# Optimization experiments

Measured on AMD Instinct MI355X. Metric: run time of the kernel, lower is better.

The kernel has to match this reference:

```python
import jax, jax.numpy as jnp
import numpy as np

B, S, DIM = 4, 2048, 1024


def _xavier(key, shape):
    # xavier_uniform for a [out, in] Linear weight
    fan_in, fan_out = shape[1], shape[0]
    limit = float(np.sqrt(6.0 / (fan_in + fan_out)))
    return jax.random.uniform(key, shape, jnp.float32, -limit, limit)


def setup_inputs() -> dict:
    key = jax.random.key(0)
    ks = jax.random.split(key, 8)
    z_real = jax.random.normal(ks[0], (B, S, DIM), jnp.float32)
    z_imag = jax.random.normal(ks[1], (B, S, DIM), jnp.float32)
    wq_r = _xavier(ks[2], (DIM, DIM))
    wq_i = _xavier(ks[3], (DIM, DIM))
    wk_r = _xavier(ks[4], (DIM, DIM))
    wk_i = _xavier(ks[5], (DIM, DIM))
    wv_r = _xavier(ks[6], (DIM, DIM))
    wv_i = _xavier(ks[7], (DIM, DIM))
    # causal mask (0 = masked), broadcast over batch
    mask = jnp.tril(jnp.ones((S, S), jnp.int32))
    return {"z_real": z_real, "z_imag": z_imag,
            "wq_r": wq_r, "wq_i": wq_i,
            "wk_r": wk_r, "wk_i": wk_i,
            "wv_r": wv_r, "wv_i": wv_i,
            "mask": mask}


def _complex_linear(xr, xi, wr, wi):
    # torch Linear: y = x @ W^T
    yr = xr @ wr.T - xi @ wi.T
    yi = xi @ wr.T + xr @ wi.T
    return yr, yi


def reference(z_real, z_imag, wq_r, wq_i, wk_r, wk_i, wv_r, wv_i, mask):
    dim = z_real.shape[-1]
    scale = dim ** (-0.5)
    qr, qi = _complex_linear(z_real, z_imag, wq_r, wq_i)
    kr, ki = _complex_linear(z_real, z_imag, wk_r, wk_i)
    vr, vi = _complex_linear(z_real, z_imag, wv_r, wv_i)
    # cat([q.real, q.imag]) @ cat([k.real, k.imag])^T == qr@kr^T + qi@ki^T
    scores = (jnp.einsum('bsd,btd->bst', qr, kr)
              + jnp.einsum('bsd,btd->bst', qi, ki)) * scale  # [B,S,S]
    scores = jnp.where(mask == 0, -jnp.inf, scores)
    attn = jax.nn.softmax(scores, axis=-1)
    out_r = jnp.einsum('bst,btd->bsd', attn, vr)
    out_i = jnp.einsum('bst,btd->bsd', attn, vi)
    return jnp.stack([out_r, out_i], axis=0)  # [2,B,S,dim] = (real, imag)
```

## Files before the change

kernel.cpp:

```cpp
#include <hip/hip_runtime.h>
#include <hip/hip_bf16.h>
#include <hip/hip_fp16.h>

#define DIMK 1024
#define SEQ  2048
#define BATCH 4
#define NTOK (BATCH*SEQ)
#define PROJ_ELEMS ((size_t)NTOK*DIMK)
#define LD 2048

typedef unsigned short ushort_t;
typedef __attribute__((ext_vector_type(8))) short short8;
typedef __attribute__((ext_vector_type(4))) float float4v;

#define MFMA_BF16 __builtin_amdgcn_mfma_f32_16x16x32_bf16

__device__ __forceinline__ unsigned short f2bf(float f) {
    union { float f; unsigned int i; } x; x.f = f;
    unsigned int r = x.i + 0x7fffu + ((x.i >> 16) & 1u);
    return (unsigned short)(r >> 16);
}

__device__ __forceinline__ void gld_lds16(const void* g, void* l) {
    auto gp = reinterpret_cast<const __attribute__((address_space(1))) unsigned int*>(
        reinterpret_cast<uintptr_t>(g));
    auto lp = reinterpret_cast<__attribute__((address_space(3))) unsigned int*>(
        reinterpret_cast<uintptr_t>(l));
    __builtin_amdgcn_global_load_lds(gp, lp, 16, 0, 0);
}

__device__ __forceinline__ void stage2(const ushort_t* __restrict__ gbase,
                                       ushort_t* lbase, int kcol,
                                       int rg0, int g, int scol)
{
    gld_lds16(gbase + (size_t)(rg0 * 16 + g) * LD + kcol + scol,
              lbase + rg0 * 512);
    gld_lds16(gbase + (size_t)(rg0 * 16 + 16 + g) * LD + kcol + scol,
              lbase + rg0 * 512 + 512);
}

__device__ __forceinline__ void gemm_core256(
    const ushort_t* __restrict__ Arow,
    const ushort_t* __restrict__ Brow,
    int kend,
    ushort_t* Alds, ushort_t* Blds,
    float4v acc[8][4], int wid, int lane)
{
    const int g    = lane >> 2;
    const int sx   = lane & 3;
    const int scol = ((sx - (g >> 1)) & 3) * 8;
    const int r16  = lane & 15;
    const int quad = lane >> 4;
    const int roff = r16 * 32 + ((quad + (r16 >> 1)) & 3) * 8;
    const int wm8 = (wid >> 2) * 8;
    const int wn4 = (wid & 3) * 4;
    const int rg0 = wid * 2;
    const int NT = kend >> 6;

    stage2(Brow, Blds,        0,  rg0, g, scol);
    stage2(Arow, Alds,        0,  rg0, g, scol);
    stage2(Brow, Blds + 8192, 32, rg0, g, scol);
    stage2(Arow, Alds + 8192, 32, rg0, g, scol);
    asm volatile("s_waitcnt vmcnt(4)" ::: "memory");
    __builtin_amdgcn_s_barrier();

    for (int t = 0; t < NT; ++t) {
        const int d     = (t & 1) << 14;
        const int dn    = d ^ 16384;
        const int knext = (t + 1) << 6;
        const bool pre  = (t + 1 < NT);
        short8 af0[4], af1[4], bf[4];

        #pragma unroll
        for (int j = 0; j < 4; ++j)
            bf[j] = *(const short8*)(Blds + d + (wn4 + j) * 512 + roff);
        #pragma unroll
        for (int i = 0; i < 4; ++i)
            af0[i] = *(const short8*)(Alds + d + (wm8 + i) * 512 + roff);
        #pragma unroll
        for (int i = 0; i < 4; ++i)
            af1[i] = *(const short8*)(Alds + d + (wm8 + 4 + i) * 512 + roff);
        if (pre) {
            stage2(Brow, Blds + dn, knext, rg0, g, scol);
            stage2(Arow, Alds + dn, knext, rg0, g, scol);
        }
        __builtin_amdgcn_s_setprio(1);
        #pragma unroll
        for (int i = 0; i < 4; ++i)
            #pragma unroll
            for (int j = 0; j < 4; ++j)
                acc[i][j] = MFMA_BF16(af0[i], bf[j], acc[i][j], 0, 0, 0);
        #pragma unroll
        for (int i = 0; i < 4; ++i)
            #pragma unroll
            for (int j = 0; j < 4; ++j)
                acc[4 + i][j] = MFMA_BF16(af1[i], bf[j], acc[4 + i][j], 0, 0, 0);
        __builtin_amdgcn_s_setprio(0);
        if (pre) asm volatile("s_waitcnt vmcnt(4)" ::: "memory");
        else     asm volatile("s_waitcnt vmcnt(0)" ::: "memory");
        __builtin_amdgcn_s_barrier();

        #pragma unroll
        for (int j = 0; j < 4; ++j)
            bf[j] = *(const short8*)(Blds + d + 8192 + (wn4 + j) * 512 + roff);
        #pragma unroll
        for (int i = 0; i < 4; ++i)
            af0[i] = *(const short8*)(Alds + d + 8192 + (wm8 + i) * 512 + roff);
        #pragma unroll
        for (int i = 0; i < 4; ++i)
            af1[i] = *(const short8*)(Alds + d + 8192 + (wm8 + 4 + i) * 512 + roff);
        if (pre) {
            stage2(Brow, Blds + dn + 8192, knext + 32, rg0, g, scol);
            stage2(Arow, Alds + dn + 8192, knext + 32, rg0, g, scol);
        }
        __builtin_amdgcn_s_setprio(1);
        #pragma unroll
        for (int i = 0; i < 4; ++i)
            #pragma unroll
            for (int j = 0; j < 4; ++j)
                acc[i][j] = MFMA_BF16(af0[i], bf[j], acc[i][j], 0, 0, 0);
        #pragma unroll
        for (int i = 0; i < 4; ++i)
            #pragma unroll
            for (int j = 0; j < 4; ++j)
                acc[4 + i][j] = MFMA_BF16(af1[i], bf[j], acc[4 + i][j], 0, 0, 0);
        __builtin_amdgcn_s_setprio(0);
        if (pre) asm volatile("s_waitcnt vmcnt(4)" ::: "memory");
        __builtin_amdgcn_s_barrier();
    }
}

__global__ __launch_bounds__(512, 2)
void gemm_proj(const ushort_t* __restrict__ A, const ushort_t* __restrict__ B,
               ushort_t* __restrict__ Cq, ushort_t* __restrict__ Ck,
               ushort_t* __restrict__ Cv)
{
    __shared__ ushort_t smem[65536];
    const int tid = threadIdx.x, wid = tid >> 6, lane = tid & 63;
    const int m0 = blockIdx.y * 256;
    const int n0g = blockIdx.x * 256;
    ushort_t* C = (n0g < 2048) ? Cq : ((n0g < 4096) ? Ck : Cv);
    const int n0 = n0g & 2047;
    float4v acc[8][4] = {};
    gemm_core256(A + (size_t)m0 * LD, B + (size_t)n0g * LD, 2048,
                 smem, smem + 32768, acc, wid, lane);

    const int wm = wid >> 2, wn = wid & 3;
    const int col16 = lane & 15, quad = lane >> 4;
    #pragma unroll
    for (int i = 0; i < 8; ++i)
        #pragma unroll
        for (int j = 0; j < 4; ++j) {
            const int n = n0 + wn * 64 + j * 16 + col16;
            #pragma unroll
            for (int r = 0; r < 4; ++r) {
                const int m = m0 + wm * 128 + i * 16 + quad * 4 + r;
                C[(size_t)m * LD + n] = f2bf(acc[i][j][r]);
            }
        }
}

__global__ __launch_bounds__(512, 2)
void gemm_scores(const ushort_t* __restrict__ Q, const ushort_t* __restrict__ K,
                 __half* __restrict__ S)
{
    const int jt = blockIdx.x, it = blockIdx.y, b = blockIdx.z;
    if (jt > it) return;
    __shared__ ushort_t smem[65536];
    const int tid = threadIdx.x, wid = tid >> 6, lane = tid & 63;
    const size_t boff = (size_t)b * SEQ * LD;
    float4v acc[8][4] = {};
    gemm_core256(Q + boff + (size_t)it * 256 * LD, K + boff + (size_t)jt * 256 * LD,
                 2048, smem, smem + 32768, acc, wid, lane);

    const int wm = wid >> 2, wn = wid & 3;
    const int col16 = lane & 15, quad = lane >> 4;
    const float scale = 0.03125f;
    __half* Sb = S + (size_t)b * SEQ * SEQ;
    #pragma unroll
    for (int i = 0; i < 8; ++i)
        #pragma unroll
        for (int j = 0; j < 4; ++j) {
            const int t = jt * 256 + wn * 64 + j * 16 + col16;
            #pragma unroll
            for (int r = 0; r < 4; ++r) {
                const int s = it * 256 + wm * 128 + i * 16 + quad * 4 + r;
                Sb[(size_t)s * SEQ + t] = __float2half(acc[i][j][r] * scale);
            }
        }
}

__global__ __launch_bounds__(512, 2)
void gemm_pv(const ushort_t* __restrict__ P, const ushort_t* __restrict__ VT,
             float* __restrict__ out)
{
    const int nt = blockIdx.x, mt = blockIdx.y, b = blockIdx.z;
    __shared__ ushort_t smem[65536];
    const int tid = threadIdx.x, wid = tid >> 6, lane = tid & 63;
    const int kend = (mt + 1) * 256;
    float4v acc[8][4] = {};
    gemm_core256(P + (size_t)b * SEQ * SEQ + (size_t)mt * 256 * LD,
                 VT + (size_t)b * LD * LD + (size_t)nt * 256 * LD,
                 kend, smem, smem + 32768, acc, wid, lane);

    const int wm = wid >> 2, wn = wid & 3;
    const int col16 = lane & 15, quad = lane >> 4;
    #pragma unroll
    for (int i = 0; i < 8; ++i)
        #pragma unroll
        for (int j = 0; j < 4; ++j) {
            const int n = nt * 256 + wn * 64 + j * 16 + col16;
            float* dst = out + ((n < 1024) ? 0 : PROJ_ELEMS);
            const int d = n & 1023;
            #pragma unroll
            for (int r = 0; r < 4; ++r) {
                const int s = mt * 256 + wm * 128 + i * 16 + quad * 4 + r;
                dst[((size_t)b * SEQ + s) * DIMK + d] = acc[i][j][r];
            }
        }
}

__global__ __launch_bounds__(256)
void zcat_kernel(const float* __restrict__ zr, const float* __restrict__ zi,
                 ushort_t* __restrict__ zcat)
{
    const size_t e = ((size_t)blockIdx.x * 256 + threadIdx.x) * 8;
    const size_t tok = e >> 11;
    const int c = (int)(e & 2047);
    const float* src = (c < 1024) ? (zr + tok * 1024 + c) : (zi + tok * 1024 + (c - 1024));
    float4 a = *(const float4*)src;
    float4 b = *(const float4*)(src + 4);
    ushort_t* d = zcat + e;
    d[0]=f2bf(a.x); d[1]=f2bf(a.y); d[2]=f2bf(a.z); d[3]=f2bf(a.w);
    d[4]=f2bf(b.x); d[5]=f2bf(b.y); d[6]=f2bf(b.z); d[7]=f2bf(b.w);
}

__global__ __launch_bounds__(256)
void wstack_kernel(const float* __restrict__ wr, const float* __restrict__ wi,
                   ushort_t* __restrict__ ws)
{
    const size_t e = ((size_t)blockIdx.x * 256 + threadIdx.x) * 8;
    const int n = (int)(e >> 11), c = (int)(e & 2047);
    const int n1 = n & 1023, c1 = c & 1023;
    const float* src;
    float sgn = 1.f;
    if (n < 1024) {
        if (c < 1024) src = wr + (size_t)n1 * 1024 + c1;
        else        { src = wi + (size_t)n1 * 1024 + c1; sgn = -1.f; }
    } else {
        src = ((c < 1024) ? wi : wr) + (size_t)n1 * 1024 + c1;
    }
    float4 a = *(const float4*)src;
    float4 b = *(const float4*)(src + 4);
    ushort_t* d = ws + e;
    d[0]=f2bf(sgn*a.x); d[1]=f2bf(sgn*a.y); d[2]=f2bf(sgn*a.z); d[3]=f2bf(sgn*a.w);
    d[4]=f2bf(sgn*b.x); d[5]=f2bf(sgn*b.y); d[6]=f2bf(sgn*b.z); d[7]=f2bf(sgn*b.w);
}

__global__ __launch_bounds__(256)
void transpose_v(const ushort_t* __restrict__ vcat, ushort_t* __restrict__ vt)
{
    __shared__ ushort_t tile[64][65];
    const int b = blockIdx.z;
    const int t0 = blockIdx.x * 64, c0 = blockIdx.y * 64;
    const int tid = threadIdx.x;
    const int r = tid >> 4, c4 = (tid & 15) * 4;
    const ushort_t* src = vcat + ((size_t)(b * SEQ + t0)) * LD + c0;
    #pragma unroll
    for (int p = 0; p < 4; ++p) {
        const int row = p * 16 + r;
        ushort4 v = *(const ushort4*)(src + (size_t)row * LD + c4);
        tile[row][c4+0]=v.x; tile[row][c4+1]=v.y; tile[row][c4+2]=v.z; tile[row][c4+3]=v.w;
    }
    __syncthreads();
    ushort_t* dst = vt + ((size_t)b * LD + c0) * LD + t0;
    #pragma unroll
    for (int p = 0; p < 4; ++p) {
        const int crow = p * 16 + r;
        ushort4 v;
        v.x = tile[c4+0][crow]; v.y = tile[c4+1][crow];
        v.z = tile[c4+2][crow]; v.w = tile[c4+3][crow];
        *(ushort4*)(dst + (size_t)crow * LD + c4) = v;
    }
}

__global__ __launch_bounds__(256)
void softmax_kernel(__half* __restrict__ sc)
{
    const int row = blockIdx.x;
    const int s = row & (SEQ - 1);
    __half* x = sc + (size_t)row * SEQ;
    ushort_t* xo = (ushort_t*)x;
    const int n = s + 1;
    const int tid = threadIdx.x, wave = tid >> 6, lane = tid & 63;
    __shared__ float redm[4], reds[4];

    float m = -1e30f;
    for (int i = tid; i < n; i += 256) m = fmaxf(m, __half2float(x[i]));
    #pragma unroll
    for (int off = 32; off > 0; off >>= 1) m = fmaxf(m, __shfl_down(m, off, 64));
    if (lane == 0) redm[wave] = m;
    __syncthreads();
    if (tid == 0) redm[0] = fmaxf(fmaxf(redm[0], redm[1]), fmaxf(redm[2], redm[3]));
    __syncthreads();
    m = redm[0];

    float l = 0.f;
    for (int i = tid; i < n; i += 256) l += __expf(__half2float(x[i]) - m);
    #pragma unroll
    for (int off = 32; off > 0; off >>= 1) l += __shfl_down(l, off, 64);
    if (lane == 0) reds[wave] = l;
    __syncthreads();
    if (tid == 0) reds[0] = reds[0] + reds[1] + reds[2] + reds[3];
    __syncthreads();
    const float inv = 1.0f / reds[0];

    const int npad = min(SEQ, ((s >> 8) + 1) << 8);
    for (int i = tid; i < npad; i += 256) {
        float v = (i < n) ? __expf(__half2float(x[i]) - m) * inv : 0.f;
        xo[i] = f2bf(v);
    }
}

extern "C" void kernel_launch(void* const* d_in, const int* in_sizes, int n_in,
                              void* d_out, int out_size, void* d_ws, size_t ws_size,
                              hipStream_t stream)
{
    const float* z_real = (const float*)d_in[0];
    const float* z_imag = (const float*)d_in[1];
    const float* wq_r   = (const float*)d_in[2];
    const float* wq_i   = (const float*)d_in[3];
    const float* wk_r   = (const float*)d_in[4];
    const float* wk_i   = (const float*)d_in[5];
    const float* wv_r   = (const float*)d_in[6];
    const float* wv_i   = (const float*)d_in[7];

    uint8_t* ws = (uint8_t*)d_ws;
    ushort_t* zcat = (ushort_t*)(ws + 0);
    ushort_t* wall = (ushort_t*)(ws + 33554432);
    ushort_t* wsq  = wall;
    ushort_t* wsk  = (ushort_t*)(ws + 33554432 + 8388608);
    ushort_t* wsv  = (ushort_t*)(ws + 33554432 + 16777216);
    ushort_t* qcat = (ushort_t*)(ws + 58720256);
    ushort_t* kcat = (ushort_t*)(ws + 92274688);
    ushort_t* vcat = (ushort_t*)(ws + 125829120);
    ushort_t* vt   = (ushort_t*)(ws + 0);
    __half*   sc   = (__half*)(ws + 125829120);
    float*    outp = (float*)d_out;

    zcat_kernel<<<dim3(8192), dim3(256), 0, stream>>>(z_real, z_imag, zcat);
    wstack_kernel<<<dim3(2048), dim3(256), 0, stream>>>(wq_r, wq_i, wsq);
    wstack_kernel<<<dim3(2048), dim3(256), 0, stream>>>(wk_r, wk_i, wsk);
    wstack_kernel<<<dim3(2048), dim3(256), 0, stream>>>(wv_r, wv_i, wsv);

    gemm_proj<<<dim3(24, 32), dim3(512), 0, stream>>>(zcat, wall, qcat, kcat, vcat);

    transpose_v<<<dim3(32, 32, 4), dim3(256), 0, stream>>>(vcat, vt);
    gemm_scores<<<dim3(8, 8, 4), dim3(512), 0, stream>>>(qcat, kcat, sc);
    softmax_kernel<<<dim3(NTOK), dim3(256), 0, stream>>>(sc);
    gemm_pv<<<dim3(8, 8, 4), dim3(512), 0, stream>>>((ushort_t*)sc, vt, outp);
}
```

Before: 473.0 us.

## Deepen GEMM K-pipeline to four LDS stages with register prefetch of next fragments

Replaces the double-buffered 64-wide K loop with a four-slot ring of 32-wide LDS stages, keeping two stages of global loads in flight. Each half-step also reads the next stage's B and low-A fragments into registers before its MFMAs, so LDS reads overlap compute and there is one barrier per 32-wide step. This is meant to hide global and LDS latency in the projection GEMM. In exchange it needs extra registers for the prefetched fragments, which could cause spills at launch bounds 512x2, and the hand-written prologue and epilogue must match the stage count exactly.

```diff
diff --git a/kernel.cpp b/kernel.cpp
--- a/kernel.cpp
+++ b/kernel.cpp
@@ -55,79 +55,96 @@
     const int wm8 = (wid >> 2) * 8;
     const int wn4 = (wid & 3) * 4;
     const int rg0 = wid * 2;
-    const int NT = kend >> 6;
-
-    stage2(Brow, Blds,        0,  rg0, g, scol);
-    stage2(Arow, Alds,        0,  rg0, g, scol);
-    stage2(Brow, Blds + 8192, 32, rg0, g, scol);
-    stage2(Arow, Alds + 8192, 32, rg0, g, scol);
+    const int L = kend >> 5;
+
+    auto STAGE = [&](int X) {
+        const int sl = (X & 3) * 8192;
+        const int kc = X * 32;
+        stage2(Brow, Blds + sl, kc, rg0, g, scol);
+        stage2(Arow, Alds + sl, kc, rg0, g, scol);
+    };
+
+    short8 bc[4], alo[4], bn[4], aln[4], ahi[4];
+
+#define READ_AHI(C)                                                         \
+    _Pragma("unroll")                                                       \
+    for (int i = 0; i < 4; ++i)                                             \
+        ahi[i] = *(const short8*)(Alds + (C) * 8192 + (wm8 + 4 + i) * 512 + roff);
+
+#define READ_NXT(N)                                                         \
+    _Pragma("unroll")                                                       \
+    for (int j = 0; j < 4; ++j)                                             \
+        bn[j] = *(const short8*)(Blds + (N) * 8192 + (wn4 + j) * 512 + roff); \
+    _Pragma("unroll")                                                       \
+    for (int i = 0; i < 4; ++i)                                             \
+        aln[i] = *(const short8*)(Alds + (N) * 8192 + (wm8 + i) * 512 + roff);
+
+#define MFMA32()                                                            \
+    __builtin_amdgcn_s_setprio(1);                                          \
+    _Pragma("unroll")                                                       \
+    for (int i = 0; i < 4; ++i)                                             \
+        _Pragma("unroll")                                                   \
+        for (int j = 0; j < 4; ++j)                                         \
+            acc[i][j] = MFMA_BF16(alo[i], bc[j], acc[i][j], 0, 0, 0);       \
+    _Pragma("unroll")                                                       \
+    for (int i = 0; i < 4; ++i)                                             \
+        _Pragma("unroll")                                                   \
+        for (int j = 0; j < 4; ++j)                                         \
+            acc[4 + i][j] = MFMA_BF16(ahi[i], bc[j], acc[4 + i][j], 0, 0, 0); \
+    __builtin_amdgcn_s_setprio(0);
+
+#define ROTATE()                                                            \
+    _Pragma("unroll")                                                       \
+    for (int q = 0; q < 4; ++q) { bc[q] = bn[q]; alo[q] = aln[q]; }
+
+#define HALF_MAIN(C, N, Xst)                                                \
+    READ_AHI(C)                                                             \
+    READ_NXT(N)                                                             \
+    STAGE(Xst);                                                             \
+    MFMA32()                                                                \
+    asm volatile("s_waitcnt vmcnt(4)" ::: "memory");                        \
+    __builtin_amdgcn_s_barrier();                                           \
+    asm volatile("" ::: "memory");                                          \
+    ROTATE()
+
+    STAGE(0); STAGE(1); STAGE(2);
     asm volatile("s_waitcnt vmcnt(4)" ::: "memory");
     __builtin_amdgcn_s_barrier();
-
-    for (int t = 0; t < NT; ++t) {
-        const int d     = (t & 1) << 14;
-        const int dn    = d ^ 16384;
-        const int knext = (t + 1) << 6;
-        const bool pre  = (t + 1 < NT);
-        short8 af0[4], af1[4], bf[4];
-
-        #pragma unroll
-        for (int j = 0; j < 4; ++j)
-            bf[j] = *(const short8*)(Blds + d + (wn4 + j) * 512 + roff);
-        #pragma unroll
-        for (int i = 0; i < 4; ++i)
-            af0[i] = *(const short8*)(Alds + d + (wm8 + i) * 512 + roff);
-        #pragma unroll
-        for (int i = 0; i < 4; ++i)
-            af1[i] = *(const short8*)(Alds + d + (wm8 + 4 + i) * 512 + roff);
-        if (pre) {
-            stage2(Brow, Blds + dn, knext, rg0, g, scol);
-            stage2(Arow, Alds + dn, knext, rg0, g, scol);
-        }
-        __builtin_amdgcn_s_setprio(1);
-        #pragma unroll
-        for (int i = 0; i < 4; ++i)
-            #pragma unroll
-            for (int j = 0; j < 4; ++j)
-                acc[i][j] = MFMA_BF16(af0[i], bf[j], acc[i][j], 0, 0, 0);
-        #pragma unroll
-        for (int i = 0; i < 4; ++i)
-            #pragma unroll
-            for (int j = 0; j < 4; ++j)
-                acc[4 + i][j] = MFMA_BF16(af1[i], bf[j], acc[4 + i][j], 0, 0, 0);
-        __builtin_amdgcn_s_setprio(0);
-        if (pre) asm volatile("s_waitcnt vmcnt(4)" ::: "memory");
-        else     asm volatile("s_waitcnt vmcnt(0)" ::: "memory");
-        __builtin_amdgcn_s_barrier();
-
-        #pragma unroll
-        for (int j = 0; j < 4; ++j)
-            bf[j] = *(const short8*)(Blds + d + 8192 + (wn4 + j) * 512 + roff);
-        #pragma unroll
-        for (int i = 0; i < 4; ++i)
-            af0[i] = *(const short8*)(Alds + d + 8192 + (wm8 + i) * 512 + roff);
-        #pragma unroll
-        for (int i = 0; i < 4; ++i)
-            af1[i] = *(const short8*)(Alds + d + 8192 + (wm8 + 4 + i) * 512 + roff);
-        if (pre) {
-            stage2(Brow, Blds + dn + 8192, knext + 32, rg0, g, scol);
-            stage2(Arow, Alds + dn + 8192, knext + 32, rg0, g, scol);
-        }
-        __builtin_amdgcn_s_setprio(1);
-        #pragma unroll
-        for (int i = 0; i < 4; ++i)
-            #pragma unroll
-            for (int j = 0; j < 4; ++j)
-                acc[i][j] = MFMA_BF16(af0[i], bf[j], acc[i][j], 0, 0, 0);
-        #pragma unroll
-        for (int i = 0; i < 4; ++i)
-            #pragma unroll
-            for (int j = 0; j < 4; ++j)
-                acc[4 + i][j] = MFMA_BF16(af1[i], bf[j], acc[4 + i][j], 0, 0, 0);
-        __builtin_amdgcn_s_setprio(0);
-        if (pre) asm volatile("s_waitcnt vmcnt(4)" ::: "memory");
-        __builtin_amdgcn_s_barrier();
-    }
+    asm volatile("" ::: "memory");
+    #pragma unroll
+    for (int j = 0; j < 4; ++j)
+        bc[j] = *(const short8*)(Blds + (wn4 + j) * 512 + roff);
+    #pragma unroll
+    for (int i = 0; i < 4; ++i)
+        alo[i] = *(const short8*)(Alds + (wm8 + i) * 512 + roff);
+
+    for (int H = 0; H + 7 < L; H += 4) {
+        HALF_MAIN(0, 1, H + 3)
+        HALF_MAIN(1, 2, H + 4)
+        HALF_MAIN(2, 3, H + 5)
+        HALF_MAIN(3, 0, H + 6)
+    }
+
+    HALF_MAIN(0, 1, L - 1)
+    READ_AHI(1)
+    READ_NXT(2)
+    MFMA32()
+    asm volatile("s_waitcnt vmcnt(0)" ::: "memory");
+    __builtin_amdgcn_s_barrier();
+    asm volatile("" ::: "memory");
+    ROTATE()
+    READ_AHI(2)
+    READ_NXT(3)
+    MFMA32()
+    ROTATE()
+    READ_AHI(3)
+    MFMA32()
+
+#undef READ_AHI
+#undef READ_NXT
+#undef MFMA32
+#undef ROTATE
+#undef HALF_MAIN
 }
 
 __global__ __launch_bounds__(512, 2)
```

Measured after the change: 487.9 us. 3.2% more time.

## Switch GEMMs to 256x128 tiles with 4 waves and single-stage K loop

Applied to the files above, without the earlier changes.

Replaces the 256x256, 8-wave GEMM core with a 256x128, 4-wave core that stages 32-wide K slices through a two-buffer LDS ring and waits for loads to finish every iteration. All three GEMM kernels move to the smaller tile, doubling grid size for better CU fill and finer causal skipping in the scores kernel. The PV kernel also reverses row-tile order for half the batches to balance causal work. The cost is less data reuse per tile and a shallower prefetch pipeline, so there are more barriers per FLOP.

```diff
diff --git a/kernel.cpp b/kernel.cpp
--- a/kernel.cpp
+++ b/kernel.cpp
@@ -39,7 +39,7 @@
               lbase + rg0 * 512 + 512);
 }
 
-__device__ __forceinline__ void gemm_core256(
+__device__ __forceinline__ void gemm_core128(
     const ushort_t* __restrict__ Arow,
     const ushort_t* __restrict__ Brow,
     int kend,
@@ -52,100 +52,64 @@
     const int r16  = lane & 15;
     const int quad = lane >> 4;
     const int roff = r16 * 32 + ((quad + (r16 >> 1)) & 3) * 8;
-    const int wm8 = (wid >> 2) * 8;
-    const int wn4 = (wid & 3) * 4;
-    const int rg0 = wid * 2;
-    const int NT = kend >> 6;
-
-    stage2(Brow, Blds,        0,  rg0, g, scol);
-    stage2(Arow, Alds,        0,  rg0, g, scol);
-    stage2(Brow, Blds + 8192, 32, rg0, g, scol);
-    stage2(Arow, Alds + 8192, 32, rg0, g, scol);
-    asm volatile("s_waitcnt vmcnt(4)" ::: "memory");
+    const int wm8 = (wid >> 1) * 8;
+    const int wn4 = (wid & 1) * 4;
+    const int rgA = wid * 4;
+    const int rgB = wid * 2;
+    const int L = kend >> 5;
+
+    auto STAGE = [&](int H) {
+        const int sa = (H & 1) * 8192, sb = (H & 1) * 4096;
+        const int kc = H * 32;
+        stage2(Arow, Alds + sa, kc, rgA,     g, scol);
+        stage2(Arow, Alds + sa, kc, rgA + 2, g, scol);
+        stage2(Brow, Blds + sb, kc, rgB,     g, scol);
+    };
+
+    STAGE(0);
+    asm volatile("s_waitcnt vmcnt(0)" ::: "memory");
     __builtin_amdgcn_s_barrier();
-
-    for (int t = 0; t < NT; ++t) {
-        const int d     = (t & 1) << 14;
-        const int dn    = d ^ 16384;
-        const int knext = (t + 1) << 6;
-        const bool pre  = (t + 1 < NT);
-        short8 af0[4], af1[4], bf[4];
-
+    asm volatile("" ::: "memory");
+
+    for (int H = 0; H < L; ++H) {
+        const int sa = (H & 1) * 8192, sb = (H & 1) * 4096;
+        short8 af[8], bf[4];
         #pragma unroll
         for (int j = 0; j < 4; ++j)
-            bf[j] = *(const short8*)(Blds + d + (wn4 + j) * 512 + roff);
-        #pragma unroll
-        for (int i = 0; i < 4; ++i)
-            af0[i] = *(const short8*)(Alds + d + (wm8 + i) * 512 + roff);
-        #pragma unroll
-        for (int i = 0; i < 4; ++i)
-            af1[i] = *(const short8*)(Alds + d + (wm8 + 4 + i) * 512 + roff);
-        if (pre) {
-            stage2(Brow, Blds + dn, knext, rg0, g, scol);
-            stage2(Arow, Alds + dn, knext, rg0, g, scol);
-        }
+            bf[j] = *(const short8*)(Blds + sb + (wn4 + j) * 512 + roff);
+        #pragma unroll
+        for (int i = 0; i < 8; ++i)
+            af[i] = *(const short8*)(Alds + sa + (wm8 + i) * 512 + roff);
+        if (H + 1 < L) STAGE(H + 1);
         __builtin_amdgcn_s_setprio(1);
         #pragma unroll
-        for (int i = 0; i < 4; ++i)
+        for (int i = 0; i < 8; ++i)
             #pragma unroll
             for (int j = 0; j < 4; ++j)
-                acc[i][j] = MFMA_BF16(af0[i], bf[j], acc[i][j], 0, 0, 0);
-        #pragma unroll
-        for (int i = 0; i < 4; ++i)
-            #pragma unroll
-            for (int j = 0; j < 4; ++j)
-                acc[4 + i][j] = MFMA_BF16(af1[i], bf[j], acc[4 + i][j], 0, 0, 0);
+                acc[i][j] = MFMA_BF16(af[i], bf[j], acc[i][j], 0, 0, 0);
         __builtin_amdgcn_s_setprio(0);
-        if (pre) asm volatile("s_waitcnt vmcnt(4)" ::: "memory");
-        else     asm volatile("s_waitcnt vmcnt(0)" ::: "memory");
+        asm volatile("s_waitcnt vmcnt(0)" ::: "memory");
         __builtin_amdgcn_s_barrier();
-
-        #pragma unroll
-        for (int j = 0; j < 4; ++j)
-            bf[j] = *(const short8*)(Blds + d + 8192 + (wn4 + j) * 512 + roff);
-        #pragma unroll
-        for (int i = 0; i < 4; ++i)
-            af0[i] = *(const short8*)(Alds + d + 8192 + (wm8 + i) * 512 + roff);
-        #pragma unroll
-        for (int i = 0; i < 4; ++i)
-            af1[i] = *(const short8*)(Alds + d + 8192 + (wm8 + 4 + i) * 512 + roff);
-        if (pre) {
-            stage2(Brow, Blds + dn + 8192, knext + 32, rg0, g, scol);
-            stage2(Arow, Alds + dn + 8192, knext + 32, rg0, g, scol);
-        }
-        __builtin_amdgcn_s_setprio(1);
-        #pragma unroll
-        for (int i = 0; i < 4; ++i)
-            #pragma unroll
-            for (int j = 0; j < 4; ++j)
-                acc[i][j] = MFMA_BF16(af0[i], bf[j], acc[i][j], 0, 0, 0);
-        #pragma unroll
-        for (int i = 0; i < 4; ++i)
-            #pragma unroll
-            for (int j = 0; j < 4; ++j)
-                acc[4 + i][j] = MFMA_BF16(af1[i], bf[j], acc[4 + i][j], 0, 0, 0);
-        __builtin_amdgcn_s_setprio(0);
-        if (pre) asm volatile("s_waitcnt vmcnt(4)" ::: "memory");
-        __builtin_amdgcn_s_barrier();
-    }
-}
-
-__global__ __launch_bounds__(512, 2)
+        asm volatile("" ::: "memory");
+    }
+}
+
+__global__ __launch_bounds__(256, 2)
 void gemm_proj(const ushort_t* __restrict__ A, const ushort_t* __restrict__ B,
                ushort_t* __restrict__ Cq, ushort_t* __restrict__ Ck,
                ushort_t* __restrict__ Cv)
 {
-    __shared__ ushort_t smem[65536];
+    __shared__ ushort_t smem[24576];
     const int tid = threadIdx.x, wid = tid >> 6, lane = tid & 63;
     const int m0 = blockIdx.y * 256;
-    const int n0g = blockIdx.x * 256;
+    const int n0g = blockIdx.x * 128;
     ushort_t* C = (n0g < 2048) ? Cq : ((n0g < 4096) ? Ck : Cv);
     const int n0 = n0g & 2047;
     float4v acc[8][4] = {};
-    gemm_core256(A + (size_t)m0 * LD, B + (size_t)n0g * LD, 2048,
-                 smem, smem + 32768, acc, wid, lane);
-
-    const int wm = wid >> 2, wn = wid & 3;
+    gemm_core128(A + (size_t)m0 * LD, B + (size_t)n0g * LD, 2048,
+                 smem, smem + 16384, acc, wid, lane);
+
+    const int wm = wid >> 1, wn = wid & 1;
     const int col16 = lane & 15, quad = lane >> 4;
     #pragma unroll
     for (int i = 0; i < 8; ++i)
@@ -160,20 +124,20 @@
         }
 }
 
-__global__ __launch_bounds__(512, 2)
+__global__ __launch_bounds__(256, 2)
 void gemm_scores(const ushort_t* __restrict__ Q, const ushort_t* __restrict__ K,
                  __half* __restrict__ S)
 {
     const int jt = blockIdx.x, it = blockIdx.y, b = blockIdx.z;
-    if (jt > it) return;
-    __shared__ ushort_t smem[65536];
+    if (jt > 2 * it + 1) return;
+    __shared__ ushort_t smem[24576];
     const int tid = threadIdx.x, wid = tid >> 6, lane = tid & 63;
     const size_t boff = (size_t)b * SEQ * LD;
     float4v acc[8][4] = {};
-    gemm_core256(Q + boff + (size_t)it * 256 * LD, K + boff + (size_t)jt * 256 * LD,
-                 2048, smem, smem + 32768, acc, wid, lane);
-
-    const int wm = wid >> 2, wn = wid & 3;
+    gemm_core128(Q + boff + (size_t)it * 256 * LD, K + boff + (size_t)jt * 128 * LD,
+                 2048, smem, smem + 16384, acc, wid, lane);
+
+    const int wm = wid >> 1, wn = wid & 1;
     const int col16 = lane & 15, quad = lane >> 4;
     const float scale = 0.03125f;
     __half* Sb = S + (size_t)b * SEQ * SEQ;
@@ -181,7 +145,7 @@
     for (int i = 0; i < 8; ++i)
         #pragma unroll
         for (int j = 0; j < 4; ++j) {
-            const int t = jt * 256 + wn * 64 + j * 16 + col16;
+            const int t = jt * 128 + wn * 64 + j * 16 + col16;
             #pragma unroll
             for (int r = 0; r < 4; ++r) {
                 const int s = it * 256 + wm * 128 + i * 16 + quad * 4 + r;
@@ -190,26 +154,27 @@
         }
 }
 
-__global__ __launch_bounds__(512, 2)
+__global__ __launch_bounds__(256, 2)
 void gemm_pv(const ushort_t* __restrict__ P, const ushort_t* __restrict__ VT,
              float* __restrict__ out)
 {
-    const int nt = blockIdx.x, mt = blockIdx.y, b = blockIdx.z;
-    __shared__ ushort_t smem[65536];
+    const int nt = blockIdx.x, b = blockIdx.z;
+    const int mt = (b >= 2) ? (7 - blockIdx.y) : blockIdx.y;
+    __shared__ ushort_t smem[24576];
     const int tid = threadIdx.x, wid = tid >> 6, lane = tid & 63;
     const int kend = (mt + 1) * 256;
     float4v acc[8][4] = {};
-    gemm_core256(P + (size_t)b * SEQ * SEQ + (size_t)mt * 256 * LD,
-                 VT + (size_t)b * LD * LD + (size_t)nt * 256 * LD,
-                 kend, smem, smem + 32768, acc, wid, lane);
-
-    const int wm = wid >> 2, wn = wid & 3;
+    gemm_core128(P + (size_t)b * SEQ * SEQ + (size_t)mt * 256 * LD,
+                 VT + (size_t)b * LD * LD + (size_t)nt * 128 * LD,
+                 kend, smem, smem + 16384, acc, wid, lane);
+
+    const int wm = wid >> 1, wn = wid & 1;
     const int col16 = lane & 15, quad = lane >> 4;
     #pragma unroll
     for (int i = 0; i < 8; ++i)
         #pragma unroll
         for (int j = 0; j < 4; ++j) {
-            const int n = nt * 256 + wn * 64 + j * 16 + col16;
+            const int n = nt * 128 + wn * 64 + j * 16 + col16;
             float* dst = out + ((n < 1024) ? 0 : PROJ_ELEMS);
             const int d = n & 1023;
             #pragma unroll
@@ -353,10 +318,10 @@
     wstack_kernel<<<dim3(2048), dim3(256), 0, stream>>>(wk_r, wk_i, wsk);
     wstack_kernel<<<dim3(2048), dim3(256), 0, stream>>>(wv_r, wv_i, wsv);
 
-    gemm_proj<<<dim3(24, 32), dim3(512), 0, stream>>>(zcat, wall, qcat, kcat, vcat);
+    gemm_proj<<<dim3(48, 32), dim3(256), 0, stream>>>(zcat, wall, qcat, kcat, vcat);
 
     transpose_v<<<dim3(32, 32, 4), dim3(256), 0, stream>>>(vcat, vt);
-    gemm_scores<<<dim3(8, 8, 4), dim3(512), 0, stream>>>(qcat, kcat, sc);
+    gemm_scores<<<dim3(16, 8, 4), dim3(256), 0, stream>>>(qcat, kcat, sc);
     softmax_kernel<<<dim3(NTOK), dim3(256), 0, stream>>>(sc);
-    gemm_pv<<<dim3(8, 8, 4), dim3(512), 0, stream>>>((ushort_t*)sc, vt, outp);
-}
+    gemm_pv<<<dim3(16, 8, 4), dim3(256), 0, stream>>>((ushort_t*)sc, vt, outp);
+}
```

Measured after the change: 532.3 us. +12.5%, slower.
